# Kernel optimization log

Hardware: AMD Instinct MI355X
Metric: run time of the kernel (lower is better)

The kernel has to match this reference:

```python
import jax, jax.numpy as jnp
import numpy as np

B, NPG, NFEAT, NHID, NCLASS = 32, 256, 128, 64, 6
N = B * NPG
E_PER = NPG * 16
C = 1.0
SQC = 1.0  # sqrt(c)
MIN_NORM = 1e-15
PROJ_EPS = 4e-3
LAMB = 1.0


def _norm(x):
    return jnp.clip(jnp.linalg.norm(x, axis=-1, keepdims=True), MIN_NORM)


def artanh(x):
    x = jnp.clip(x, -1.0 + 1e-7, 1.0 - 1e-7)
    return 0.5 * (jnp.log1p(x) - jnp.log1p(-x))


def proj(x):
    # clip points to stay inside the Poincare ball
    n = _norm(x)
    maxn = (1.0 - PROJ_EPS) / SQC
    return jnp.where(n > maxn, x / n * maxn, x)


def expmap0(u):
    un = _norm(u)
    return jnp.tanh(SQC * un) * u / (SQC * un)


def logmap0(p):
    pn = _norm(p)
    return artanh(SQC * pn) * p / (SQC * pn)


def mobius_matvec(W, x):
    xn = _norm(x)
    mx = x @ W.T
    mxn = _norm(mx)
    return jnp.tanh(mxn / xn * artanh(SQC * xn)) * mx / (mxn * SQC)


def mobius_add(x, y):
    x2 = jnp.sum(x * x, -1, keepdims=True)
    y2 = jnp.sum(y * y, -1, keepdims=True)
    xy = jnp.sum(x * y, -1, keepdims=True)
    num = (1.0 + 2.0 * C * xy + C * y2) * x + (1.0 - C * x2) * y
    den = 1.0 + 2.0 * C * xy + C * C * x2 * y2
    return num / jnp.clip(den, MIN_NORM)


def hgc_layer(xh, adj, W, b):
    # HypLinear (mobius matvec + hyperbolic bias)
    h = proj(mobius_matvec(W, xh))
    hb = proj(expmap0(b.reshape(1, -1)))
    h = proj(mobius_add(h, hb))
    # HypAgg: aggregate in tangent space at origin
    h = proj(expmap0(adj @ logmap0(h)))
    # HypAct: relu in tangent space
    return proj(expmap0(jax.nn.relu(logmap0(h))))


def hgpsl_pool(x, adj, att, nb, npg):
    deg = adj.sum(-1)
    dis = jnp.where(deg > 0, deg ** -0.5, 0.0)
    prop = dis[:, None] * (adj @ (dis[:, None] * x))
    score = jnp.abs(x - prop).sum(-1)  # [N]
    k = npg // 2
    vals, idx = jax.lax.top_k(score.reshape(nb, npg), k)  # per-graph top-k
    gidx = (idx + (jnp.arange(nb) * npg)[:, None]).reshape(-1)  # global ids
    xn = x[gidx] * jnp.tanh(vals).reshape(-1, 1)
    adj_ind = adj[gidx][:, gidx]
    # structure learning: single-head additive attention, masked per graph
    d = xn.shape[-1]
    e = jax.nn.leaky_relu((xn @ att[:d])[:, None] + (xn @ att[d:])[None, :], 0.2)
    gid = jnp.repeat(jnp.arange(nb), k)
    mask = gid[:, None] == gid[None, :]
    new_adj = jnp.where(mask, jax.nn.relu(e) + LAMB * adj_ind, 0.0)
    return xn, new_adj


def readout(x, nb, k):
    xr = x.reshape(nb, k, -1)
    return jnp.concatenate([xr.max(axis=1), xr.mean(axis=1)], axis=-1)


def to_hyp(t):
    return proj(expmap0(t))  # proj_tan0 is identity on the Poincare ball


def forward(x, edge_index, W1, b1, W2, b2, W3, b3, att1, att2,
            lw1, lb1, lw2, lb2, lw3, lb3):
    row, col = edge_index[0], edge_index[1]
    w = (x[row].sum(-1) + x[col].sum(-1)) * 0.5
    adj1 = jnp.zeros((N, N), x.dtype).at[row, col].set(w)

    t = logmap0(hgc_layer(to_hyp(x), adj1, W1, b1))
    t, adj2 = hgpsl_pool(t, adj1, att1, B, NPG)
    k1 = NPG // 2
    x1 = readout(t, B, k1)

    t = logmap0(hgc_layer(to_hyp(t), adj2, W2, b2))
    t, adj3 = hgpsl_pool(t, adj2, att2, B, k1)
    k2 = k1 // 2
    x2 = readout(t, B, k2)

    t = logmap0(hgc_layer(to_hyp(t), adj3, W3, b3))
    x3 = readout(t, B, k2)

    r = jax.nn.relu(x1) + jax.nn.relu(x2) + jax.nn.relu(x3)
    r = jax.nn.relu(r @ lw1.T + lb1)
    r = jax.nn.relu(r @ lw2.T + lb2)
    return jax.nn.log_softmax(r @ lw3.T + lb3, axis=-1)


def setup_inputs() -> dict:
    key = jax.random.key(0)
    ks = jax.random.split(key, 16)
    s = 0.1
    x = jax.random.normal(ks[0], (N, NFEAT), jnp.float32)
    off = jnp.repeat(jnp.arange(B, dtype=jnp.int32) * NPG, E_PER)
    row = jax.random.randint(ks[1], (B * E_PER,), 0, NPG, jnp.int32) + off
    col = jax.random.randint(ks[2], (B * E_PER,), 0, NPG, jnp.int32) + off
    edge_index = jnp.stack([row, col])
    return {
        "x": x,
        "edge_index": edge_index,
        "W1": jax.random.normal(ks[3], (NHID, NFEAT), jnp.float32) * s,
        "b1": jax.random.normal(ks[4], (NHID,), jnp.float32) * s,
        "W2": jax.random.normal(ks[5], (NHID, NHID), jnp.float32) * s,
        "b2": jax.random.normal(ks[6], (NHID,), jnp.float32) * s,
        "W3": jax.random.normal(ks[7], (NHID, NHID), jnp.float32) * s,
        "b3": jax.random.normal(ks[8], (NHID,), jnp.float32) * s,
        "att1": jax.random.normal(ks[9], (2 * NHID,), jnp.float32) * s,
        "att2": jax.random.normal(ks[10], (2 * NHID,), jnp.float32) * s,
        "lw1": jax.random.normal(ks[11], (NHID, 2 * NHID), jnp.float32) * s,
        "lb1": jnp.zeros((NHID,), jnp.float32),
        "lw2": jax.random.normal(ks[12], (NHID // 2, NHID), jnp.float32) * s,
        "lb2": jnp.zeros((NHID // 2,), jnp.float32),
        "lw3": jax.random.normal(ks[13], (NCLASS, NHID // 2), jnp.float32) * s,
        "lb3": jnp.zeros((NCLASS,), jnp.float32),
    }


def reference(x, edge_index, W1, b1, W2, b2, W3, b3, att1, att2,
              lw1, lb1, lw2, lb2, lw3, lb3):
    return forward(x, edge_index, W1, b1, W2, b2, W3, b3, att1, att2,
                   lw1, lb1, lw2, lb2, lw3, lb3)
```

## Files before the change

### kernel.cpp

```cpp
#include <hip/hip_runtime.h>
#include <math.h>

#define MAXN 0.996f

__device__ __forceinline__ float wredsum(float v) {
#pragma unroll
  for (int o = 32; o > 0; o >>= 1) v += __shfl_xor(v, o);
  return v;
}

__device__ __forceinline__ float artanh_f(float x) {
  x = fminf(fmaxf(x, -1.0f + 1e-7f), 1.0f - 1e-7f);
  return 0.5f * (log1pf(x) - log1pf(-x));
}

__device__ __forceinline__ float cload(const float* p) {
  return __hip_atomic_load(p, __ATOMIC_RELAXED, __HIP_MEMORY_SCOPE_AGENT);
}
__device__ __forceinline__ int cloadi(const int* p) {
  return __hip_atomic_load(p, __ATOMIC_RELAXED, __HIP_MEMORY_SCOPE_AGENT);
}
__device__ __forceinline__ void cstore(float* p, float v) {
  __hip_atomic_store(p, v, __ATOMIC_RELAXED, __HIP_MEMORY_SCOPE_AGENT);
}
__device__ __forceinline__ void cstorei(int* p, int v) {
  __hip_atomic_store(p, v, __ATOMIC_RELAXED, __HIP_MEMORY_SCOPE_AGENT);
}

template <int N>
__device__ __forceinline__ void stageN(float* dst, const float* src, int tid) {
  float v[N];
#pragma unroll
  for (int k = 0; k < N; ++k) v[k] = cload(src + tid + k * 1024);
#pragma unroll
  for (int k = 0; k < N; ++k) dst[tid + k * 1024] = v[k];
}

__device__ __forceinline__ float chainB(float acc) {
  float n0 = sqrtf(wredsum(acc * acc));
  float u0 = fmaxf(n0, 1e-15f);
  float e1 = tanhf(u0) / u0;
  float c1 = fmaxf(e1 * n0, 1e-15f);
  float v = acc * e1;
  if (c1 > MAXN) { v *= MAXN / c1; c1 = MAXN; }
  v *= artanh_f(c1) / c1;
  v = fmaxf(v, 0.f);
  float n2 = sqrtf(wredsum(v * v));
  float u2 = fmaxf(n2, 1e-15f);
  float e2 = tanhf(u2) / u2;
  float c2 = fmaxf(e2 * n2, 1e-15f);
  v *= e2;
  if (c2 > MAXN) { v *= MAXN / c2; c2 = MAXN; }
  v *= artanh_f(c2) / c2;
  return v;
}

__device__ __forceinline__ void hbCalc(int j, const float* __restrict__ b,
                                       float& hbj, float& y2) {
  float bj = b[j];
  float nb = sqrtf(wredsum(bj * bj));
  float ub = fmaxf(nb, 1e-15f);
  float eb = tanhf(ub) / ub;
  float cb = fmaxf(eb * nb, 1e-15f);
  hbj = bj * eb * ((cb > MAXN) ? MAXN / cb : 1.0f);
  y2 = wredsum(hbj * hbj);
}

template <int IND>
__device__ __forceinline__ void doArow(int j, const float* xs, const float* wT,
                                       float hbj, float y2,
                                       float* __restrict__ uout) {
  float a2 = xs[j] * xs[j];
  if (IND == 128) { float x1v = xs[64 + j]; a2 += x1v * x1v; }
  float nx = sqrtf(wredsum(a2));
  float un = fmaxf(nx, 1e-15f);
  float s1 = tanhf(un) / un;
  float nv = s1 * nx;
  float nn = fmaxf(nv, 1e-15f);
  float s2 = (nn > MAXN) ? MAXN / nn : 1.0f;
  float alpha = s1 * s2;
  float xn = fmaxf(fminf(nn, MAXN), 1e-15f);

  float y = 0.f;
  for (int t = 0; t < IND; ++t) y = fmaf(xs[t], wT[t * 65 + j], y);
  float mxj = alpha * y;
  float mxn = fmaxf(sqrtf(wredsum(mxj * mxj)), 1e-15f);
  float hj = (tanhf(mxn / xn * artanh_f(xn)) / mxn) * mxj;

  float hn = fmaxf(sqrtf(wredsum(hj * hj)), 1e-15f);
  if (hn > MAXN) hj *= MAXN / hn;

  float x2 = wredsum(hj * hj);
  float xy = wredsum(hj * hbj);
  float num = (1.f + 2.f * xy + y2) * hj + (1.f - x2) * hbj;
  float den = fmaxf(1.f + 2.f * xy + x2 * y2, 1e-15f);
  float aj = num / den;

  float an = fmaxf(sqrtf(wredsum(aj * aj)), 1e-15f);
  float pn = an;
  if (an > MAXN) { aj *= MAXN / an; pn = MAXN; }
  cstore(uout + j, (artanh_f(pn) / pn) * aj);
}

template <int NP, int TR, bool WANTDIS>
__device__ __forceinline__ void doBgrpL(int j, int r0, int r0l,
                                        const float* adjS, const float* uS,
                                        float* __restrict__ tg,
                                        float* __restrict__ disg) {
  float acc[TR], dsum[TR];
#pragma unroll
  for (int r = 0; r < TR; ++r) { acc[r] = 0.f; dsum[r] = 0.f; }
  for (int c0 = 0; c0 < NP; c0 += 4) {
    float uv0 = uS[(c0 + 0) * 64 + j];
    float uv1 = uS[(c0 + 1) * 64 + j];
    float uv2 = uS[(c0 + 2) * 64 + j];
    float uv3 = uS[(c0 + 3) * 64 + j];
#pragma unroll
    for (int r = 0; r < TR; ++r) {
      const float4 a4 = *(const float4*)(adjS + (r0l + r) * NP + c0);
      acc[r] = fmaf(a4.x, uv0, acc[r]);
      acc[r] = fmaf(a4.y, uv1, acc[r]);
      acc[r] = fmaf(a4.z, uv2, acc[r]);
      acc[r] = fmaf(a4.w, uv3, acc[r]);
      if (WANTDIS) {
        dsum[r] += a4.x; dsum[r] += a4.y; dsum[r] += a4.z; dsum[r] += a4.w;
      }
    }
  }
#pragma unroll
  for (int r = 0; r < TR; ++r) {
    float v = chainB(acc[r]);
    cstore(tg + (size_t)(r0 + r) * 64 + j, v);
    if (WANTDIS && j == 0)
      cstore(disg + r0 + r, (dsum[r] > 0.f) ? (1.0f / sqrtf(dsum[r])) : 0.f);
  }
}

template <int NP, int TR>
__device__ __forceinline__ void doCgrpL(int j, int r0, int r0l,
                                        const float* adjS, const float* prodS,
                                        const float* disS,
                                        const float* __restrict__ tg,
                                        float* __restrict__ scoreg) {
  float acc[TR];
#pragma unroll
  for (int r = 0; r < TR; ++r) acc[r] = 0.f;
  for (int c0 = 0; c0 < NP; c0 += 4) {
    float uv0 = prodS[(c0 + 0) * 64 + j];
    float uv1 = prodS[(c0 + 1) * 64 + j];
    float uv2 = prodS[(c0 + 2) * 64 + j];
    float uv3 = prodS[(c0 + 3) * 64 + j];
#pragma unroll
    for (int r = 0; r < TR; ++r) {
      const float4 a4 = *(const float4*)(adjS + (r0l + r) * NP + c0);
      acc[r] = fmaf(a4.x, uv0, acc[r]);
      acc[r] = fmaf(a4.y, uv1, acc[r]);
      acc[r] = fmaf(a4.z, uv2, acc[r]);
      acc[r] = fmaf(a4.w, uv3, acc[r]);
    }
  }
#pragma unroll
  for (int r = 0; r < TR; ++r) {
    float tval = cload(tg + (size_t)(r0 + r) * 64 + j);
    float d = fabsf(tval - disS[r0 + r] * acc[r]);
    d = wredsum(d);
    if (j == 0) cstore(scoreg + r0 + r, d);
  }
}

template <int NP>
__device__ __forceinline__ void doDEa(int j, int i, const float* scS,
                                      const float* __restrict__ tg,
                                      const float* __restrict__ att,
                                      float* __restrict__ xng,
                                      float* __restrict__ s1g,
                                      float* __restrict__ s2g,
                                      int* __restrict__ selg) {
  constexpr int K = NP / 2;
  float si = scS[i];
  float cnt = 0.f;
#pragma unroll
  for (int kk = 0; kk < NP / 64; ++kk) {
    int c = j + kk * 64;
    float v = scS[c];
    cnt += ((v > si) || (v == si && c < i)) ? 1.f : 0.f;
  }
  int rank = (int)wredsum(cnt);
  if (rank < K) {
    float tv = tanhf(si);
    float v = cload(tg + (size_t)i * 64 + j) * tv;
    cstore(xng + (size_t)rank * 64 + j, v);
    float a = wredsum(v * att[j]);
    float b2 = wredsum(v * att[64 + j]);
    if (j == 0) {
      cstore(s1g + rank, a);
      cstore(s2g + rank, b2);
      cstorei(selg + rank, i);
    }
  }
}

template <int K>
__device__ __forceinline__ void doReadout(int j, const float* __restrict__ xng,
                                          float* __restrict__ xrg) {
  float mx = -1e30f, sm = 0.f;
#pragma unroll
  for (int r = 0; r < K; ++r) {
    float v = cload(xng + (size_t)r * 64 + j);
    mx = fmaxf(mx, v);
    sm += v;
  }
  cstore(xrg + j, mx);
  cstore(xrg + 64 + j, sm * (1.0f / K));
}

__device__ __forceinline__ void cluster_bar(int* bar, int target, int tid) {
  __syncthreads();
  if (tid == 0) {
    __hip_atomic_fetch_add(bar, 1, __ATOMIC_RELAXED, __HIP_MEMORY_SCOPE_AGENT);
    while (__hip_atomic_load(bar, __ATOMIC_RELAXED, __HIP_MEMORY_SCOPE_AGENT) <
           target * 8)
      __builtin_amdgcn_s_sleep(2);
  }
  __syncthreads();
}

struct KP {
  const float* x; const int* ei; int nE;
  const float *W1, *b1, *W2, *b2, *W3, *b3, *att1, *att2;
  const float *lw1, *lb1, *lw2, *lb2, *lw3, *lb3;
  float *adj1, *adj2, *adj3, *srow, *ubuf, *t1, *t2, *t3, *dis, *score;
  float *xn1, *xn2, *s1b, *s2b, *x1, *x2;
  int *sel, *bar;
  float* out;
};

__global__ void __launch_bounds__(1024, 4) k_fwd(KP P) {
  const int tid = threadIdx.x;
  const int wib = tid >> 6;
  const int j = tid & 63;
  const int g = blockIdx.x >> 3;
  const int lb = blockIdx.x & 7;
  const int wc = lb * 16 + wib;
  const int tc = lb * 1024 + tid;

  __shared__ float wT[128 * 65];
  __shared__ float xsAll[16 * 128];
  __shared__ float stage[16384];
  __shared__ float adjS[8192];
  __shared__ float scS[256];
  __shared__ float s1S[128];
  __shared__ float s2S[128];
  __shared__ int selS[128];
  float* xs = xsAll + wib * 128;

  int* bar = P.bar + g * 64;
  float* adj1g = P.adj1 + (size_t)g * 65536;
  float* adj2g = P.adj2 + (size_t)g * 16384;
  float* adj3g = P.adj3 + (size_t)g * 4096;
  const float* xg = P.x + (size_t)g * 32768;
  float* srowg = P.srow + g * 256;
  float* ubufg = P.ubuf + (size_t)g * 16384;
  float* t1g = P.t1 + (size_t)g * 16384;
  float* t2g = P.t2 + (size_t)g * 8192;
  float* t3g = P.t3 + (size_t)g * 4096;
  float* disg = P.dis + g * 256;
  float* scoreg = P.score + g * 256;
  float* xn1g = P.xn1 + (size_t)g * 8192;
  float* xn2g = P.xn2 + (size_t)g * 4096;
  float* s1g = P.s1b + g * 128;
  float* s2g = P.s2b + g * 128;
  int* selg = P.sel + g * 128;
  float* x1g = P.x1 + g * 128;
  float* x2g = P.x2 + g * 128;

  {
#pragma unroll
    for (int k = 0; k < 8; ++k) cstore(adj1g + tc + k * 8192, 0.f);
    for (int row = wc; row < 256; row += 128) {
      float a = xg[(size_t)row * 128 + j] + xg[(size_t)row * 128 + 64 + j];
      a = wredsum(a);
      if (j == 0) cstore(srowg + row, a);
    }
    for (int idx = tid; idx < 8192; idx += 1024)
      wT[(idx & 127) * 65 + (idx >> 7)] = P.W1[idx];
  }
  cluster_bar(bar, 1, tid);

  {
    if (tid < 256) scS[tid] = cload(srowg + tid);
    __syncthreads();
    const int epg = P.nE >> 5;
    for (int e = g * epg + tc; e < (g + 1) * epg; e += 8192) {
      int r = P.ei[e] & 255, c = P.ei[P.nE + e] & 255;
      cstore(adj1g + r * 256 + c, 0.5f * (scS[r] + scS[c]));
    }
    float hbj, y2;
    hbCalc(j, P.b1, hbj, y2);
    for (int row = wc; row < 256; row += 128) {
      xs[j] = xg[(size_t)row * 128 + j];
      xs[64 + j] = xg[(size_t)row * 128 + 64 + j];
      doArow<128>(j, xs, wT, hbj, y2, ubufg + (size_t)row * 64);
    }
  }
  cluster_bar(bar, 2, tid);

  {
    stageN<8>(adjS, adj1g + lb * 8192, tid);
    stageN<16>(stage, ubufg, tid);
    __syncthreads();
    doBgrpL<256, 2, true>(j, wc * 2, wib * 2, adjS, stage, t1g, disg);
    for (int idx = tid; idx < 4096; idx += 1024)
      wT[(idx & 63) * 65 + (idx >> 6)] = P.W2[idx];
  }
  cluster_bar(bar, 3, tid);

  {
    if (tid < 256) scS[tid] = cload(disg + tid);
    __syncthreads();
    {
      float v[16];
#pragma unroll
      for (int k = 0; k < 16; ++k) {
        int idx = tid + k * 1024;
        v[k] = cload(t1g + idx) * scS[idx >> 6];
      }
#pragma unroll
      for (int k = 0; k < 16; ++k) stage[tid + k * 1024] = v[k];
    }
    __syncthreads();
    doCgrpL<256, 2>(j, wc * 2, wib * 2, adjS, stage, scS, t1g, scoreg);
  }
  cluster_bar(bar, 4, tid);

  {
    if (tid < 256) scS[tid] = cload(scoreg + tid);
    __syncthreads();
    for (int row = wc; row < 256; row += 128)
      doDEa<256>(j, row, scS, t1g, P.att1, xn1g, s1g, s2g, selg);
  }
  cluster_bar(bar, 5, tid);

  {
    if (tid < 128) {
      s1S[tid] = cload(s1g + tid);
      s2S[tid] = cload(s2g + tid);
      selS[tid] = cloadi(selg + tid);
    }
    __syncthreads();
    for (int idx = tc; idx < 16384; idx += 8192) {
      int ii = idx >> 7, jj = idx & 127;
      cstore(adj2g + idx, fmaxf(s1S[ii] + s2S[jj], 0.f) +
                              cload(adj1g + selS[ii] * 256 + selS[jj]));
    }
    if (wc == 0) doReadout<128>(j, xn1g, x1g);
    float hbj, y2;
    hbCalc(j, P.b2, hbj, y2);
    {
      int row = wc;
      xs[j] = cload(xn1g + (size_t)row * 64 + j);
      doArow<64>(j, xs, wT, hbj, y2, ubufg + (size_t)row * 64);
    }
  }
  cluster_bar(bar, 6, tid);

  {
    stageN<2>(adjS, adj2g + lb * 2048, tid);
    stageN<8>(stage, ubufg, tid);
    __syncthreads();
    doBgrpL<128, 1, true>(j, wc, wib, adjS, stage, t2g, disg);
    for (int idx = tid; idx < 4096; idx += 1024)
      wT[(idx & 63) * 65 + (idx >> 6)] = P.W3[idx];
  }
  cluster_bar(bar, 7, tid);

  {
    if (tid < 128) scS[tid] = cload(disg + tid);
    __syncthreads();
    {
      float v[8];
#pragma unroll
      for (int k = 0; k < 8; ++k) {
        int idx = tid + k * 1024;
        v[k] = cload(t2g + idx) * scS[idx >> 6];
      }
#pragma unroll
      for (int k = 0; k < 8; ++k) stage[tid + k * 1024] = v[k];
    }
    __syncthreads();
    doCgrpL<128, 1>(j, wc, wib, adjS, stage, scS, t2g, scoreg);
  }
  cluster_bar(bar, 8, tid);

  {
    if (tid < 128) scS[tid] = cload(scoreg + tid);
    __syncthreads();
    doDEa<128>(j, wc, scS, t2g, P.att2, xn2g, s1g, s2g, selg);
  }
  cluster_bar(bar, 9, tid);

  {
    if (tid < 64) {
      s1S[tid] = cload(s1g + tid);
      s2S[tid] = cload(s2g + tid);
      selS[tid] = cloadi(selg + tid);
    }
    __syncthreads();
    if (tc < 4096) {
      int ii = tc >> 6, jj = tc & 63;
      cstore(adj3g + tc, fmaxf(s1S[ii] + s2S[jj], 0.f) +
                             cload(adj2g + selS[ii] * 128 + selS[jj]));
    }
    if (wc == 0) doReadout<64>(j, xn2g, x2g);
    float hbj, y2;
    hbCalc(j, P.b3, hbj, y2);
    if (wc < 64) {
      int row = wc;
      xs[j] = cload(xn2g + (size_t)row * 64 + j);
      doArow<64>(j, xs, wT, hbj, y2, ubufg + (size_t)row * 64);
    }
  }
  cluster_bar(bar, 10, tid);

  if (lb < 4) {
    adjS[tid] = cload(adj3g + lb * 1024 + tid);
    stageN<4>(stage, ubufg, tid);
    __syncthreads();
    doBgrpL<64, 1, false>(j, wc, wib, adjS, stage, t3g, nullptr);
  }
  cluster_bar(bar, 11, tid);

  if (wc == 0) {
    float mx = -1e30f, sm = 0.f;
#pragma unroll
    for (int r = 0; r < 64; ++r) {
      float v = cload(t3g + (size_t)r * 64 + j);
      mx = fmaxf(mx, v);
      sm += v;
    }
    float* S = xsAll;
    S[j] = fmaxf(cload(x1g + j), 0.f) + fmaxf(cload(x2g + j), 0.f) +
           fmaxf(mx, 0.f);
    S[64 + j] = fmaxf(cload(x1g + 64 + j), 0.f) +
                fmaxf(cload(x2g + 64 + j), 0.f) +
                fmaxf(sm * (1.0f / 64.0f), 0.f);
    float acc = P.lb1[j];
    for (int t = 0; t < 128; ++t) acc += S[t] * P.lw1[(size_t)j * 128 + t];
    S[128 + j] = fmaxf(acc, 0.f);
    if (j < 32) {
      float a = P.lb2[j];
      for (int t = 0; t < 64; ++t) a += S[128 + t] * P.lw2[(size_t)j * 64 + t];
      S[192 + j] = fmaxf(a, 0.f);
    }
    if (j < 6) {
      float a = P.lb3[j];
      for (int t = 0; t < 32; ++t) a += S[192 + t] * P.lw3[(size_t)j * 32 + t];
      S[224 + j] = a;
    }
    if (j < 6) {
      float m = S[224];
      for (int c = 1; c < 6; ++c) m = fmaxf(m, S[224 + c]);
      float se = 0.f;
      for (int c = 0; c < 6; ++c) se += expf(S[224 + c] - m);
      P.out[(size_t)g * 6 + j] = S[224 + j] - m - logf(se);
    }
  }
}

extern "C" void kernel_launch(void* const* d_in, const int* in_sizes, int n_in,
                              void* d_out, int out_size, void* d_ws,
                              size_t ws_size, hipStream_t stream) {
  KP hp;
  hp.x = (const float*)d_in[0];
  hp.ei = (const int*)d_in[1];
  hp.nE = in_sizes[1] / 2;
  hp.W1 = (const float*)d_in[2];
  hp.b1 = (const float*)d_in[3];
  hp.W2 = (const float*)d_in[4];
  hp.b2 = (const float*)d_in[5];
  hp.W3 = (const float*)d_in[6];
  hp.b3 = (const float*)d_in[7];
  hp.att1 = (const float*)d_in[8];
  hp.att2 = (const float*)d_in[9];
  hp.lw1 = (const float*)d_in[10];
  hp.lb1 = (const float*)d_in[11];
  hp.lw2 = (const float*)d_in[12];
  hp.lb2 = (const float*)d_in[13];
  hp.lw3 = (const float*)d_in[14];
  hp.lb3 = (const float*)d_in[15];
  hp.out = (float*)d_out;

  float* p = (float*)d_ws;
  hp.adj1 = p;  p += (size_t)32 * 65536;
  hp.adj2 = p;  p += (size_t)32 * 16384;
  hp.adj3 = p;  p += (size_t)32 * 4096;
  hp.ubuf = p;  p += (size_t)32 * 16384;
  hp.t1 = p;    p += (size_t)32 * 16384;
  hp.t2 = p;    p += (size_t)32 * 8192;
  hp.t3 = p;    p += (size_t)32 * 4096;
  hp.srow = p;  p += 32 * 256;
  hp.dis = p;   p += 32 * 256;
  hp.score = p; p += 32 * 256;
  hp.xn1 = p;   p += (size_t)32 * 8192;
  hp.xn2 = p;   p += (size_t)32 * 4096;
  hp.s1b = p;   p += 32 * 128;
  hp.s2b = p;   p += 32 * 128;
  hp.x1 = p;    p += 32 * 128;
  hp.x2 = p;    p += 32 * 128;
  hp.sel = (int*)p; p += 32 * 128;
  hp.bar = (int*)p; p += 32 * 64;

  hipMemsetAsync(hp.bar, 0, 32 * 64 * sizeof(int), stream);
  k_fwd<<<256, 1024, 0, stream>>>(hp);
}
```

Baseline: 222.0 us.

## Keep adjacency slices in LDS, drop global adj1 and one cluster barrier

Each block now builds its own 32-row slice of the first-level adjacency directly in shared memory, with each block computing all row sums itself. This removes the global adj1 buffer, its zeroing, the srow buffer and one cross-block cluster barrier. The pooled adjacency gather now reads from the LDS slice owned by the block. Stage C reuses the staged t tile for the dis-scaled products and for the top-k gather, and global stores and loads are widened to 64-bit pairs. Costs are redundant row-sum work in every block and extra shuffles for the paired stores.

Result: faster. 213.0 us (-4.1%).

```diff
diff --git a/kernel.cpp b/kernel.cpp
--- a/kernel.cpp
+++ b/kernel.cpp
@@ -26,14 +26,27 @@
 __device__ __forceinline__ void cstorei(int* p, int v) {
   __hip_atomic_store(p, v, __ATOMIC_RELAXED, __HIP_MEMORY_SCOPE_AGENT);
 }
-
+__device__ __forceinline__ void cstore64(float* p, float lo, float hi) {
+  unsigned long long u =
+      ((unsigned long long)__float_as_uint(hi) << 32) | __float_as_uint(lo);
+  __hip_atomic_store((unsigned long long*)p, u, __ATOMIC_RELAXED,
+                     __HIP_MEMORY_SCOPE_AGENT);
+}
+__device__ __forceinline__ void pairStore(float* base, int j, float v) {
+  float o = __shfl_xor(v, 1);
+  if ((j & 1) == 0) cstore64(base + j, v, o);
+}
 template <int N>
-__device__ __forceinline__ void stageN(float* dst, const float* src, int tid) {
-  float v[N];
-#pragma unroll
-  for (int k = 0; k < N; ++k) v[k] = cload(src + tid + k * 1024);
-#pragma unroll
-  for (int k = 0; k < N; ++k) dst[tid + k * 1024] = v[k];
+__device__ __forceinline__ void stage64(float* dst, const float* src, int tid) {
+  const unsigned long long* s = (const unsigned long long*)src;
+  unsigned long long* d = (unsigned long long*)dst;
+  unsigned long long v[N];
+#pragma unroll
+  for (int k = 0; k < N; ++k)
+    v[k] = __hip_atomic_load(s + tid + k * 1024, __ATOMIC_RELAXED,
+                             __HIP_MEMORY_SCOPE_AGENT);
+#pragma unroll
+  for (int k = 0; k < N; ++k) d[tid + k * 1024] = v[k];
 }
 
 __device__ __forceinline__ float chainB(float acc) {
@@ -99,7 +112,7 @@
   float an = fmaxf(sqrtf(wredsum(aj * aj)), 1e-15f);
   float pn = an;
   if (an > MAXN) { aj *= MAXN / an; pn = MAXN; }
-  cstore(uout + j, (artanh_f(pn) / pn) * aj);
+  pairStore(uout, j, (artanh_f(pn) / pn) * aj);
 }
 
 template <int NP, int TR, bool WANTDIS>
@@ -130,7 +143,7 @@
 #pragma unroll
   for (int r = 0; r < TR; ++r) {
     float v = chainB(acc[r]);
-    cstore(tg + (size_t)(r0 + r) * 64 + j, v);
+    pairStore(tg + (size_t)(r0 + r) * 64, j, v);
     if (WANTDIS && j == 0)
       cstore(disg + r0 + r, (dsum[r] > 0.f) ? (1.0f / sqrtf(dsum[r])) : 0.f);
   }
@@ -138,18 +151,17 @@
 
 template <int NP, int TR>
 __device__ __forceinline__ void doCgrpL(int j, int r0, int r0l,
-                                        const float* adjS, const float* prodS,
+                                        const float* adjS, const float* tS,
                                         const float* disS,
-                                        const float* __restrict__ tg,
                                         float* __restrict__ scoreg) {
   float acc[TR];
 #pragma unroll
   for (int r = 0; r < TR; ++r) acc[r] = 0.f;
   for (int c0 = 0; c0 < NP; c0 += 4) {
-    float uv0 = prodS[(c0 + 0) * 64 + j];
-    float uv1 = prodS[(c0 + 1) * 64 + j];
-    float uv2 = prodS[(c0 + 2) * 64 + j];
-    float uv3 = prodS[(c0 + 3) * 64 + j];
+    float uv0 = disS[c0 + 0] * tS[(c0 + 0) * 64 + j];
+    float uv1 = disS[c0 + 1] * tS[(c0 + 1) * 64 + j];
+    float uv2 = disS[c0 + 2] * tS[(c0 + 2) * 64 + j];
+    float uv3 = disS[c0 + 3] * tS[(c0 + 3) * 64 + j];
 #pragma unroll
     for (int r = 0; r < TR; ++r) {
       const float4 a4 = *(const float4*)(adjS + (r0l + r) * NP + c0);
@@ -161,8 +173,7 @@
   }
 #pragma unroll
   for (int r = 0; r < TR; ++r) {
-    float tval = cload(tg + (size_t)(r0 + r) * 64 + j);
-    float d = fabsf(tval - disS[r0 + r] * acc[r]);
+    float d = fabsf(tS[(r0 + r) * 64 + j] - disS[r0 + r] * acc[r]);
     d = wredsum(d);
     if (j == 0) cstore(scoreg + r0 + r, d);
   }
@@ -170,7 +181,7 @@
 
 template <int NP>
 __device__ __forceinline__ void doDEa(int j, int i, const float* scS,
-                                      const float* __restrict__ tg,
+                                      const float* tS,
                                       const float* __restrict__ att,
                                       float* __restrict__ xng,
                                       float* __restrict__ s1g,
@@ -188,8 +199,8 @@
   int rank = (int)wredsum(cnt);
   if (rank < K) {
     float tv = tanhf(si);
-    float v = cload(tg + (size_t)i * 64 + j) * tv;
-    cstore(xng + (size_t)rank * 64 + j, v);
+    float v = tS[i * 64 + j] * tv;
+    pairStore(xng + (size_t)rank * 64, j, v);
     float a = wredsum(v * att[j]);
     float b2 = wredsum(v * att[64 + j]);
     if (j == 0) {
@@ -229,7 +240,7 @@
   const float* x; const int* ei; int nE;
   const float *W1, *b1, *W2, *b2, *W3, *b3, *att1, *att2;
   const float *lw1, *lb1, *lw2, *lb2, *lw3, *lb3;
-  float *adj1, *adj2, *adj3, *srow, *ubuf, *t1, *t2, *t3, *dis, *score;
+  float *adj2, *adj3, *ubuf, *t1, *t2, *t3, *dis, *score;
   float *xn1, *xn2, *s1b, *s2b, *x1, *x2;
   int *sel, *bar;
   float* out;
@@ -242,7 +253,6 @@
   const int g = blockIdx.x >> 3;
   const int lb = blockIdx.x & 7;
   const int wc = lb * 16 + wib;
-  const int tc = lb * 1024 + tid;
 
   __shared__ float wT[128 * 65];
   __shared__ float xsAll[16 * 128];
@@ -255,11 +265,9 @@
   float* xs = xsAll + wib * 128;
 
   int* bar = P.bar + g * 64;
-  float* adj1g = P.adj1 + (size_t)g * 65536;
   float* adj2g = P.adj2 + (size_t)g * 16384;
   float* adj3g = P.adj3 + (size_t)g * 4096;
   const float* xg = P.x + (size_t)g * 32768;
-  float* srowg = P.srow + g * 256;
   float* ubufg = P.ubuf + (size_t)g * 16384;
   float* t1g = P.t1 + (size_t)g * 16384;
   float* t2g = P.t2 + (size_t)g * 8192;
@@ -275,25 +283,22 @@
   float* x2g = P.x2 + g * 128;
 
   {
-#pragma unroll
-    for (int k = 0; k < 8; ++k) cstore(adj1g + tc + k * 8192, 0.f);
-    for (int row = wc; row < 256; row += 128) {
+    for (int idx = tid; idx < 8192; idx += 1024)
+      wT[(idx & 127) * 65 + (idx >> 7)] = P.W1[idx];
+    for (int row = wib * 16; row < wib * 16 + 16; ++row) {
       float a = xg[(size_t)row * 128 + j] + xg[(size_t)row * 128 + 64 + j];
       a = wredsum(a);
-      if (j == 0) cstore(srowg + row, a);
-    }
-    for (int idx = tid; idx < 8192; idx += 1024)
-      wT[(idx & 127) * 65 + (idx >> 7)] = P.W1[idx];
-  }
-  cluster_bar(bar, 1, tid);
-
-  {
-    if (tid < 256) scS[tid] = cload(srowg + tid);
+      if (j == 0) scS[row] = a;
+    }
+    for (int k = tid; k < 8192; k += 1024) adjS[k] = 0.f;
     __syncthreads();
     const int epg = P.nE >> 5;
-    for (int e = g * epg + tc; e < (g + 1) * epg; e += 8192) {
-      int r = P.ei[e] & 255, c = P.ei[P.nE + e] & 255;
-      cstore(adj1g + r * 256 + c, 0.5f * (scS[r] + scS[c]));
+    for (int e = g * epg + tid; e < (g + 1) * epg; e += 1024) {
+      int r = P.ei[e] & 255;
+      if ((r >> 5) == lb) {
+        int c = P.ei[P.nE + e] & 255;
+        adjS[(r & 31) * 256 + c] = 0.5f * (scS[r] + scS[c]);
+      }
     }
     float hbj, y2;
     hbCalc(j, P.b1, hbj, y2);
@@ -303,43 +308,32 @@
       doArow<128>(j, xs, wT, hbj, y2, ubufg + (size_t)row * 64);
     }
   }
-  cluster_bar(bar, 2, tid);
-
-  {
-    stageN<8>(adjS, adj1g + lb * 8192, tid);
-    stageN<16>(stage, ubufg, tid);
+  cluster_bar(bar, 1, tid);
+
+  {
+    stage64<8>(stage, ubufg, tid);
     __syncthreads();
     doBgrpL<256, 2, true>(j, wc * 2, wib * 2, adjS, stage, t1g, disg);
     for (int idx = tid; idx < 4096; idx += 1024)
       wT[(idx & 63) * 65 + (idx >> 6)] = P.W2[idx];
   }
+  cluster_bar(bar, 2, tid);
+
+  {
+    if (tid < 256) scS[tid] = cload(disg + tid);
+    stage64<8>(stage, t1g, tid);
+    __syncthreads();
+    doCgrpL<256, 2>(j, wc * 2, wib * 2, adjS, stage, scS, scoreg);
+  }
   cluster_bar(bar, 3, tid);
 
   {
-    if (tid < 256) scS[tid] = cload(disg + tid);
-    __syncthreads();
-    {
-      float v[16];
-#pragma unroll
-      for (int k = 0; k < 16; ++k) {
-        int idx = tid + k * 1024;
-        v[k] = cload(t1g + idx) * scS[idx >> 6];
-      }
-#pragma unroll
-      for (int k = 0; k < 16; ++k) stage[tid + k * 1024] = v[k];
-    }
-    __syncthreads();
-    doCgrpL<256, 2>(j, wc * 2, wib * 2, adjS, stage, scS, t1g, scoreg);
+    if (tid < 256) scS[tid] = cload(scoreg + tid);
+    __syncthreads();
+    for (int row = wc; row < 256; row += 128)
+      doDEa<256>(j, row, scS, stage, P.att1, xn1g, s1g, s2g, selg);
   }
   cluster_bar(bar, 4, tid);
-
-  {
-    if (tid < 256) scS[tid] = cload(scoreg + tid);
-    __syncthreads();
-    for (int row = wc; row < 256; row += 128)
-      doDEa<256>(j, row, scS, t1g, P.att1, xn1g, s1g, s2g, selg);
-  }
-  cluster_bar(bar, 5, tid);
 
   {
     if (tid < 128) {
@@ -348,10 +342,16 @@
       selS[tid] = cloadi(selg + tid);
     }
     __syncthreads();
-    for (int idx = tc; idx < 16384; idx += 8192) {
-      int ii = idx >> 7, jj = idx & 127;
-      cstore(adj2g + idx, fmaxf(s1S[ii] + s2S[jj], 0.f) +
-                              cload(adj1g + selS[ii] * 256 + selS[jj]));
+    for (int idx2 = tid; idx2 < 8192; idx2 += 1024) {
+      int ii = idx2 >> 6, jp = idx2 & 63;
+      int sii = selS[ii];
+      if ((sii >> 5) == lb) {
+        int jj0 = jp * 2;
+        const float* arow = adjS + (sii & 31) * 256;
+        float v0 = fmaxf(s1S[ii] + s2S[jj0], 0.f) + arow[selS[jj0]];
+        float v1 = fmaxf(s1S[ii] + s2S[jj0 + 1], 0.f) + arow[selS[jj0 + 1]];
+        cstore64(adj2g + ii * 128 + jj0, v0, v1);
+      }
     }
     if (wc == 0) doReadout<128>(j, xn1g, x1g);
     float hbj, y2;
@@ -362,42 +362,32 @@
       doArow<64>(j, xs, wT, hbj, y2, ubufg + (size_t)row * 64);
     }
   }
-  cluster_bar(bar, 6, tid);
-
-  {
-    stageN<2>(adjS, adj2g + lb * 2048, tid);
-    stageN<8>(stage, ubufg, tid);
+  cluster_bar(bar, 5, tid);
+
+  {
+    stage64<1>(adjS, adj2g + lb * 2048, tid);
+    stage64<4>(stage, ubufg, tid);
     __syncthreads();
     doBgrpL<128, 1, true>(j, wc, wib, adjS, stage, t2g, disg);
     for (int idx = tid; idx < 4096; idx += 1024)
       wT[(idx & 63) * 65 + (idx >> 6)] = P.W3[idx];
   }
+  cluster_bar(bar, 6, tid);
+
+  {
+    if (tid < 128) scS[tid] = cload(disg + tid);
+    stage64<4>(stage, t2g, tid);
+    __syncthreads();
+    doCgrpL<128, 1>(j, wc, wib, adjS, stage, scS, scoreg);
+  }
   cluster_bar(bar, 7, tid);
 
   {
-    if (tid < 128) scS[tid] = cload(disg + tid);
-    __syncthreads();
-    {
-      float v[8];
-#pragma unroll
-      for (int k = 0; k < 8; ++k) {
-        int idx = tid + k * 1024;
-        v[k] = cload(t2g + idx) * scS[idx >> 6];
-      }
-#pragma unroll
-      for (int k = 0; k < 8; ++k) stage[tid + k * 1024] = v[k];
-    }
-    __syncthreads();
-    doCgrpL<128, 1>(j, wc, wib, adjS, stage, scS, t2g, scoreg);
+    if (tid < 128) scS[tid] = cload(scoreg + tid);
+    __syncthreads();
+    doDEa<128>(j, wc, scS, stage, P.att2, xn2g, s1g, s2g, selg);
   }
   cluster_bar(bar, 8, tid);
-
-  {
-    if (tid < 128) scS[tid] = cload(scoreg + tid);
-    __syncthreads();
-    doDEa<128>(j, wc, scS, t2g, P.att2, xn2g, s1g, s2g, selg);
-  }
-  cluster_bar(bar, 9, tid);
 
   {
     if (tid < 64) {
@@ -406,10 +396,16 @@
       selS[tid] = cloadi(selg + tid);
     }
     __syncthreads();
-    if (tc < 4096) {
-      int ii = tc >> 6, jj = tc & 63;
-      cstore(adj3g + tc, fmaxf(s1S[ii] + s2S[jj], 0.f) +
-                             cload(adj2g + selS[ii] * 128 + selS[jj]));
+    for (int idx2 = tid; idx2 < 2048; idx2 += 1024) {
+      int ii = idx2 >> 5, jp = idx2 & 31;
+      int sii = selS[ii];
+      if ((sii >> 4) == lb) {
+        int jj0 = jp * 2;
+        const float* arow = adjS + (sii & 15) * 128;
+        float v0 = fmaxf(s1S[ii] + s2S[jj0], 0.f) + arow[selS[jj0]];
+        float v1 = fmaxf(s1S[ii] + s2S[jj0 + 1], 0.f) + arow[selS[jj0 + 1]];
+        cstore64(adj3g + ii * 64 + jj0, v0, v1);
+      }
     }
     if (wc == 0) doReadout<64>(j, xn2g, x2g);
     float hbj, y2;
@@ -420,15 +416,20 @@
       doArow<64>(j, xs, wT, hbj, y2, ubufg + (size_t)row * 64);
     }
   }
+  cluster_bar(bar, 9, tid);
+
+  if (lb < 4) {
+    if (tid < 512) {
+      unsigned long long v = __hip_atomic_load(
+          (const unsigned long long*)(adj3g + lb * 1024) + tid,
+          __ATOMIC_RELAXED, __HIP_MEMORY_SCOPE_AGENT);
+      ((unsigned long long*)adjS)[tid] = v;
+    }
+    stage64<2>(stage, ubufg, tid);
+    __syncthreads();
+    doBgrpL<64, 1, false>(j, wc, wib, adjS, stage, t3g, nullptr);
+  }
   cluster_bar(bar, 10, tid);
-
-  if (lb < 4) {
-    adjS[tid] = cload(adj3g + lb * 1024 + tid);
-    stageN<4>(stage, ubufg, tid);
-    __syncthreads();
-    doBgrpL<64, 1, false>(j, wc, wib, adjS, stage, t3g, nullptr);
-  }
-  cluster_bar(bar, 11, tid);
 
   if (wc == 0) {
     float mx = -1e30f, sm = 0.f;
@@ -491,14 +492,12 @@
   hp.out = (float*)d_out;
 
   float* p = (float*)d_ws;
-  hp.adj1 = p;  p += (size_t)32 * 65536;
   hp.adj2 = p;  p += (size_t)32 * 16384;
   hp.adj3 = p;  p += (size_t)32 * 4096;
   hp.ubuf = p;  p += (size_t)32 * 16384;
   hp.t1 = p;    p += (size_t)32 * 16384;
   hp.t2 = p;    p += (size_t)32 * 8192;
   hp.t3 = p;    p += (size_t)32 * 4096;
-  hp.srow = p;  p += 32 * 256;
   hp.dis = p;   p += 32 * 256;
   hp.score = p; p += 32 * 256;
   hp.xn1 = p;   p += (size_t)32 * 8192;
```
